# Optimization experiments

Hardware: AMD Instinct MI355X
Metric: run time of the kernel (lower is better)

## Reference

```python
import jax, jax.numpy as jnp
import numpy as np

H = 16  # num_heads
D = 1024  # hidden_dim
HD = D // H  # head_dim


def setup_inputs() -> dict:
    key = jax.random.key(0)
    ks = jax.random.split(key, 12)
    B, S = 2, 2048
    x = jax.random.normal(ks[0], (B, S, D), dtype=jnp.float32)
    attention_bias = jax.random.normal(ks[1], (H, S, S), dtype=jnp.float32) * 0.1
    # padding mask: True = masked; last (S - len) positions padded, no all-masked rows
    lengths = jax.random.randint(ks[2], (B,), S // 2, S + 1)
    key_padding_mask = jnp.arange(S)[None, :] >= lengths[:, None]  # [B, S] bool
    s = 1.0 / np.sqrt(D)
    Wq = jax.random.normal(ks[3], (D, D), dtype=jnp.float32) * s
    bq = jnp.zeros((D,), dtype=jnp.float32)
    Wk = jax.random.normal(ks[4], (D, D), dtype=jnp.float32) * s
    bk = jnp.zeros((D,), dtype=jnp.float32)
    Wv = jax.random.normal(ks[5], (D, D), dtype=jnp.float32) * s
    bv = jnp.zeros((D,), dtype=jnp.float32)
    Wo = jax.random.normal(ks[6], (D, D), dtype=jnp.float32) * s
    bo = jnp.zeros((D,), dtype=jnp.float32)
    return {"x": x, "attention_bias": attention_bias, "key_padding_mask": key_padding_mask,
            "Wq": Wq, "bq": bq, "Wk": Wk, "bk": bk, "Wv": Wv, "bv": bv, "Wo": Wo, "bo": bo}


def reference(x, attention_bias, key_padding_mask, Wq, bq, Wk, bk, Wv, bv, Wo, bo):
    B, S, _ = x.shape
    scale = HD ** (-0.5)

    def shape_heads(t):  # [B,S,D] -> [B,H,S,HD]
        return t.reshape(B, S, H, HD).transpose(0, 2, 1, 3)

    q = shape_heads(x @ Wq + bq)
    k = shape_heads(x @ Wk + bk)
    v = shape_heads(x @ Wv + bv)

    attn = jnp.einsum('bhqd,bhkd->bhqk', q, k) * scale  # [B,H,S,S]
    attn = attn + attention_bias[None]
    attn = jnp.where(key_padding_mask[:, None, None, :], -jnp.inf, attn)

    # handle fully-masked rows: zero their logits pre-softmax, zero weights after
    all_masked = jnp.all(key_padding_mask, axis=1)  # [B]
    bad = all_masked[:, None, None, None]
    safe_attn = jnp.where(bad, 0.0, attn)
    weights = jax.nn.softmax(safe_attn, axis=-1)
    weights = jnp.where(bad, 0.0, weights)

    context = jnp.einsum('bhqk,bhkd->bhqd', weights, v)  # [B,H,S,HD]
    context = context.transpose(0, 2, 1, 3).reshape(B, S, D)
    return context @ Wo + bo
```

## Files before the change

kernel.cpp:

```cpp
#include <hip/hip_runtime.h>
#include <hip/hip_bf16.h>
#include <stdint.h>

#define BB 2
#define SS 2048
#define DDIM 1024
#define HH 16
#define HDIM 64

typedef __hip_bfloat16 bf16;
typedef __bf16 bf16x8 __attribute__((ext_vector_type(8)));
typedef float f32x4 __attribute__((ext_vector_type(4)));
typedef short short8 __attribute__((ext_vector_type(8)));
typedef short s16x4 __attribute__((ext_vector_type(4)));

static __device__ __forceinline__ f32x4 mfma16(bf16x8 a, bf16x8 b, f32x4 c) {
  return __builtin_amdgcn_mfma_f32_16x16x32_bf16(a, b, c, 0, 0, 0);
}

static __device__ __forceinline__ void gload_lds16(const void* g, void* l) {
  __builtin_amdgcn_global_load_lds(
      (const __attribute__((address_space(1))) void*)g,
      (__attribute__((address_space(3))) void*)l, 16, 0, 0);
}

__global__ __launch_bounds__(256) void cvt_k(const float* __restrict__ src,
                                             bf16* __restrict__ dst) {
  const int base = (blockIdx.x * 256 + threadIdx.x) * 8;
  float4 a = *reinterpret_cast<const float4*>(src + base);
  float4 b = *reinterpret_cast<const float4*>(src + base + 4);
  union {
    bf16 h[8];
    short8 v;
  } u;
  u.h[0] = __float2bfloat16(a.x);
  u.h[1] = __float2bfloat16(a.y);
  u.h[2] = __float2bfloat16(a.z);
  u.h[3] = __float2bfloat16(a.w);
  u.h[4] = __float2bfloat16(b.x);
  u.h[5] = __float2bfloat16(b.y);
  u.h[6] = __float2bfloat16(b.z);
  u.h[7] = __float2bfloat16(b.w);
  *reinterpret_cast<short8*>(dst + base) = u.v;
}

__global__ __launch_bounds__(256) void transpose_cvt4_k(
    const float* __restrict__ s0, const float* __restrict__ s1,
    const float* __restrict__ s2, const float* __restrict__ s3,
    bf16* __restrict__ d0, bf16* __restrict__ d1, bf16* __restrict__ d2,
    bf16* __restrict__ d3) {
  __shared__ float tile[64][65];
  const int zi = blockIdx.z;
  const float* src = zi == 0 ? s0 : (zi == 1 ? s1 : (zi == 2 ? s2 : s3));
  bf16* dst = zi == 0 ? d0 : (zi == 1 ? d1 : (zi == 2 ? d2 : d3));
  const int t = threadIdx.x;
  const int r = t >> 2, c0 = (t & 3) * 16;
  const int bx = blockIdx.x * 64, by = blockIdx.y * 64;
  const float* sp = src + (size_t)(by + r) * DDIM + bx + c0;
#pragma unroll
  for (int j = 0; j < 16; ++j) tile[r][c0 + j] = sp[j];
  __syncthreads();
  bf16* dp = dst + (size_t)(bx + r) * DDIM + by + c0;
#pragma unroll
  for (int j = 0; j < 16; ++j) dp[j] = __float2bfloat16(tile[c0 + j][r]);
}

__global__ __launch_bounds__(64) void mask_pack_k(
    const int* __restrict__ kpm, unsigned long long* __restrict__ mb) {
  const int i = blockIdx.x;
  const int b = i >> 5, c = i & 31;
  const unsigned long long bits =
      __ballot(kpm[b * SS + c * 64 + threadIdx.x] != 0);
  if (threadIdx.x == 0) mb[i] = bits;
}

template <int MODE>
__global__ __launch_bounds__(256, 2) void gemm_bt(
    const bf16* __restrict__ A, const bf16* __restrict__ Bt,
    const float* __restrict__ b0, const float* __restrict__ b1,
    const float* __restrict__ b2, bf16* __restrict__ O0,
    bf16* __restrict__ O1, bf16* __restrict__ O2, float* __restrict__ Of) {
  constexpr int Kd = DDIM;
  __shared__ bf16x8 lA[128 * 8];
  __shared__ bf16x8 lB[128 * 8];
  const int tid = threadIdx.x;
  const int wave = tid >> 6, lane = tid & 63;
  const int l15 = lane & 15, l4 = lane >> 4;
  const int wm = wave >> 1, wn = wave & 1;
  const int m0 = blockIdx.x * 128, n0 = blockIdx.y * 128;
  const f32x4 z = {0.f, 0.f, 0.f, 0.f};
  f32x4 acc[4][4];
#pragma unroll
  for (int i = 0; i < 4; ++i)
#pragma unroll
    for (int j = 0; j < 4; ++j) acc[i][j] = z;

  for (int k0 = 0; k0 < Kd; k0 += 64) {
#pragma unroll
    for (int j = 0; j < 4; ++j) {
      const int slot = j * 256 + tid;
      const int r = slot >> 3, cs = slot & 7;
      const int c = cs ^ (r & 7);
      gload_lds16(A + (size_t)(m0 + r) * Kd + k0 + c * 8,
                  &lA[j * 256 + wave * 64]);
      gload_lds16(Bt + (size_t)(n0 + r) * Kd + k0 + c * 8,
                  &lB[j * 256 + wave * 64]);
    }
    __syncthreads();
    bf16x8 af[2][4], bfr[2][4];
#pragma unroll
    for (int ks = 0; ks < 2; ++ks) {
#pragma unroll
      for (int i = 0; i < 4; ++i) {
        const int ra = wm * 64 + i * 16 + l15;
        af[ks][i] = lA[ra * 8 + ((ks * 4 + l4) ^ (ra & 7))];
        const int rb = wn * 64 + i * 16 + l15;
        bfr[ks][i] = lB[rb * 8 + ((ks * 4 + l4) ^ (rb & 7))];
      }
    }
#pragma unroll
    for (int ks = 0; ks < 2; ++ks)
#pragma unroll
      for (int i = 0; i < 4; ++i)
#pragma unroll
        for (int j = 0; j < 4; ++j)
          acc[i][j] = mfma16(af[ks][i], bfr[ks][j], acc[i][j]);
    __syncthreads();
  }

#pragma unroll
  for (int i = 0; i < 4; ++i) {
    const int m = m0 + wm * 64 + i * 16 + l4 * 4;
#pragma unroll
    for (int j = 0; j < 4; ++j) {
      const int n = n0 + wn * 64 + j * 16 + l15;
      if (MODE == 1) {
        const float bb = b0[n];
#pragma unroll
        for (int r = 0; r < 4; ++r)
          Of[(size_t)(m + r) * DDIM + n] = acc[i][j][r] + bb;
      } else {
        const int sel = n >> 10, nn = n & 1023;
        const int h = nn >> 6, d = nn & 63;
        const float* bp = sel == 0 ? b0 : (sel == 1 ? b1 : b2);
        const float bb = bp[nn];
        const int b = m >> 11, s = m & 2047;
        if (sel == 2) {
          union {
            bf16 h4[4];
            s16x4 v;
          } u;
#pragma unroll
          for (int r = 0; r < 4; ++r)
            u.h4[r] = __float2bfloat16(acc[i][j][r] + bb);
          *reinterpret_cast<s16x4*>(
              &O2[((size_t)(b * HH + h) * HDIM + d) * SS + s]) = u.v;
        } else {
#pragma unroll
          for (int r = 0; r < 4; ++r) {
            const float val = acc[i][j][r] + bb;
            (sel ? O1 : O0)[((size_t)(b * HH + h) * SS + (s + r)) * HDIM + d] =
                __float2bfloat16(val);
          }
        }
      }
    }
  }
}

__global__ __launch_bounds__(512, 1) void attn_k(
    const bf16* __restrict__ Qb, const bf16* __restrict__ Kb,
    const bf16* __restrict__ Vt, const float* __restrict__ bias,
    const unsigned long long* __restrict__ mbits, bf16* __restrict__ ctx) {
  __shared__ bf16x8 lK[2][512];
  __shared__ bf16x8 lV[2][512];
  __shared__ unsigned int plP[8 * 512];
  const int tid = threadIdx.x;
  const int wave = tid >> 6, lane = tid & 63;
  const int l15 = lane & 15, l4 = lane >> 4;
  const int bid = ((blockIdx.x & 7) << 6) | (blockIdx.x >> 3);
  const int qblk = bid & 15, bh = bid >> 4;
  const int b = bh >> 4, h = bh & 15;
  const int q0b = qblk * 128;
  const int q0w = q0b + wave * 16;

  const bf16* Qp = Qb + ((size_t)bh * SS + q0w) * HDIM;
  const bf16* Kp = Kb + (size_t)bh * SS * HDIM;
  const bf16* Vp = Vt + (size_t)bh * HDIM * SS;
  const float* Bp = bias + (size_t)h * SS * SS + (size_t)(q0w + l15) * SS;
  unsigned int* plw = plP + wave * 512;

  const int rs0 = tid >> 3, cs0 = (tid & 7) ^ (rs0 & 7);

  gload_lds16(Kp + (size_t)rs0 * HDIM + cs0 * 8, &lK[0][wave * 64]);
  gload_lds16(Vp + (size_t)rs0 * SS + cs0 * 8, &lV[0][wave * 64]);

  f32x4 bA0 = *reinterpret_cast<const f32x4*>(Bp + 0 * 16 + l4 * 4);
  f32x4 bA1 = *reinterpret_cast<const f32x4*>(Bp + 1 * 16 + l4 * 4);
  f32x4 bA2 = *reinterpret_cast<const f32x4*>(Bp + 2 * 16 + l4 * 4);
  f32x4 bA3 = *reinterpret_cast<const f32x4*>(Bp + 3 * 16 + l4 * 4);
  f32x4 bB0 = bA0, bB1 = bA1, bB2 = bA2, bB3 = bA3;

  bf16x8 qf[2];
#pragma unroll
  for (int ks = 0; ks < 2; ++ks)
    qf[ks] = *reinterpret_cast<const bf16x8*>(Qp + (size_t)l15 * HDIM +
                                              ks * 32 + l4 * 8);
  const f32x4 z = {0.f, 0.f, 0.f, 0.f};
  f32x4 o[4];
#pragma unroll
  for (int dd = 0; dd < 4; ++dd) o[dd] = z;
  float mrow = -1e30f, lrow = 0.f;

  __syncthreads();

#define JJROW(JJ, BC)                                                     \
  {                                                                       \
    const unsigned nib = (unsigned)(mb >> ((JJ)*16 + l4 * 4)) & 15u;      \
    _Pragma("unroll") for (int r = 0; r < 4; ++r) {                       \
      const float a = ((nib >> r) & 1u) ? -1e30f : (BC)[r];               \
      v[JJ][r] = fmaf(sc[JJ][r], 0.125f, a);                              \
      bm = fmaxf(bm, v[JJ][r]);                                           \
    }                                                                     \
  }

#define STEP(T, BC0, BC1, BC2, BC3, BN0, BN1, BN2, BN3)                        \
  {                                                                            \
    const int cur = (T)&1;                                                     \
    const int nxt = cur ^ 1;                                                   \
    const int kbn = ((T) + 1) * 64;                                            \
    const bool pf = (T) < 31;                                                  \
    if (pf) {                                                                  \
      BN0 = *reinterpret_cast<const f32x4*>(Bp + kbn + 0 * 16 + l4 * 4);       \
      BN1 = *reinterpret_cast<const f32x4*>(Bp + kbn + 1 * 16 + l4 * 4);       \
      BN2 = *reinterpret_cast<const f32x4*>(Bp + kbn + 2 * 16 + l4 * 4);       \
      BN3 = *reinterpret_cast<const f32x4*>(Bp + kbn + 3 * 16 + l4 * 4);       \
    }                                                                          \
    f32x4 sc[4];                                                               \
    __builtin_amdgcn_s_setprio(1);                                             \
    _Pragma("unroll") for (int jj = 0; jj < 4; ++jj) {                         \
      const int R = jj * 16 + l15;                                             \
      bf16x8 kf0 = lK[cur][R * 8 + ((0 + l4) ^ (R & 7))];                      \
      bf16x8 kf1 = lK[cur][R * 8 + ((4 + l4) ^ (R & 7))];                      \
      f32x4 s = mfma16(kf0, qf[0], z);                                         \
      s = mfma16(kf1, qf[1], s);                                               \
      sc[jj] = s;                                                              \
    }                                                                          \
    __builtin_amdgcn_s_setprio(0);                                             \
    if (pf) {                            \
      gload_lds16(Kp + (size_t)(kbn + rs0) * HDIM + cs0 * 8,                   \
                  &lK[nxt][wave * 64]);                                        \
    }                                                                          \
    const unsigned long long mb = mbits[(b << 5) + (T)];                       \
    float v[4][4];                                                             \
    float bm = -1e30f;                                                         \
    JJROW(0, BC0)                                                              \
    JJROW(1, BC1)                                                              \
    JJROW(2, BC2)                                                              \
    JJROW(3, BC3)                                                              \
    bm = fmaxf(bm, __shfl_xor(bm, 16));                                        \
    bm = fmaxf(bm, __shfl_xor(bm, 32));                                        \
    const bool resc = __any(bm > mrow + 8.0f);                                 \
    float alpha = 1.0f;                                                        \
    if (resc) {                                                                \
      const float mn = fmaxf(mrow, bm);                                        \
      alpha = __expf(mrow - mn);                                               \
      mrow = mn;                                                               \
    }                                                                          \
    float ps = 0.f;                                                            \
    float p[4][4];                                                             \
    _Pragma("unroll") for (int jj = 0; jj < 4; ++jj)                           \
        _Pragma("unroll") for (int r = 0; r < 4; ++r) {                        \
      p[jj][r] = __expf(v[jj][r] - mrow);                                      \
      ps += p[jj][r];                                                          \
    }                                                                          \
    ps += __shfl_xor(ps, 16);                                                  \
    ps += __shfl_xor(ps, 32);                                                  \
    lrow = lrow * alpha + ps;                                                  \
    _Pragma("unroll") for (int jj = 0; jj < 4; ++jj) {                         \
      union {                                                                  \
        bf16 h4[4];                                                            \
        unsigned long long w;                                                  \
      } u;                                                                     \
      u.h4[0] = __float2bfloat16(p[jj][0]);                                    \
      u.h4[1] = __float2bfloat16(p[jj][1]);                                    \
      u.h4[2] = __float2bfloat16(p[jj][2]);                                    \
      u.h4[3] = __float2bfloat16(p[jj][3]);                                    \
      const int byte = (l15 * 128 + jj * 32 + l4 * 8) ^ ((l15 & 7) << 4);      \
      *reinterpret_cast<unsigned long long*>(                                  \
          reinterpret_cast<char*>(plw) + byte) = u.w;                          \
    }                                                                          \
    bf16x8 vfr[4][2];                                                          \
    _Pragma("unroll") for (int dd = 0; dd < 4; ++dd) {                         \
      const int D = dd * 16 + l15;                                             \
      vfr[dd][0] = lV[cur][D * 8 + ((0 + l4) ^ (D & 7))];                      \
      vfr[dd][1] = lV[cur][D * 8 + ((4 + l4) ^ (D & 7))];                      \
    }                                                                          \
    if (pf) {                            \
      gload_lds16(Vp + (size_t)rs0 * SS + kbn + cs0 * 8,                       \
                  &lV[nxt][wave * 64]);                                        \
    }                                                                          \
    asm volatile("s_waitcnt lgkmcnt(0)" ::: "memory");                         \
    bf16x8 pfr[2];                                                             \
    _Pragma("unroll") for (int ks = 0; ks < 2; ++ks) {                         \
      const int byte = (l15 * 128 + ks * 64 + l4 * 16) ^ ((l15 & 7) << 4);     \
      pfr[ks] = *reinterpret_cast<const bf16x8*>(                              \
          reinterpret_cast<const char*>(plw) + byte);                          \
    }                                                                          \
    if (resc) {                                                                \
      float ar0 = __shfl(alpha, l4 * 4 + 0);                                   \
      float ar1 = __shfl(alpha, l4 * 4 + 1);                                   \
      float ar2 = __shfl(alpha, l4 * 4 + 2);                                   \
      float ar3 = __shfl(alpha, l4 * 4 + 3);                                   \
      _Pragma("unroll") for (int dd = 0; dd < 4; ++dd) {                       \
        o[dd][0] *= ar0;                                                       \
        o[dd][1] *= ar1;                                                       \
        o[dd][2] *= ar2;                                                       \
        o[dd][3] *= ar3;                                                       \
      }                                                                        \
    }                                                                          \
    __builtin_amdgcn_s_setprio(1);                                             \
    _Pragma("unroll") for (int dd = 0; dd < 4; ++dd) {                         \
      o[dd] = mfma16(pfr[0], vfr[dd][0], o[dd]);                               \
      o[dd] = mfma16(pfr[1], vfr[dd][1], o[dd]);                               \
    }                                                                          \
    __builtin_amdgcn_s_setprio(0);                                             \
    __syncthreads();                                                           \
  }

  for (int t2 = 0; t2 < 16; ++t2) {
    const int te = t2 * 2;
    STEP(te, bA0, bA1, bA2, bA3, bB0, bB1, bB2, bB3)
    STEP(te + 1, bB0, bB1, bB2, bB3, bA0, bA1, bA2, bA3)
  }
#undef STEP
#undef JJROW

  const float rl = 1.0f / lrow;
  float rlr[4];
#pragma unroll
  for (int r = 0; r < 4; ++r) rlr[r] = __shfl(rl, l4 * 4 + r);
#pragma unroll
  for (int dd = 0; dd < 4; ++dd) {
#pragma unroll
    for (int r = 0; r < 4; ++r) {
      const float val = o[dd][r] * rlr[r];
      const int s = q0w + l4 * 4 + r;
      ctx[((size_t)b * SS + s) * DDIM + h * HDIM + dd * 16 + l15] =
          __float2bfloat16(val);
    }
  }
}

extern "C" void kernel_launch(void* const* d_in, const int* in_sizes, int n_in,
                              void* d_out, int out_size, void* d_ws,
                              size_t ws_size, hipStream_t stream) {
  const float* x = (const float*)d_in[0];
  const float* abias = (const float*)d_in[1];
  const int* kpm = (const int*)d_in[2];
  const float* Wq = (const float*)d_in[3];
  const float* bq = (const float*)d_in[4];
  const float* Wk = (const float*)d_in[5];
  const float* bk = (const float*)d_in[6];
  const float* Wv = (const float*)d_in[7];
  const float* bv = (const float*)d_in[8];
  const float* Wo = (const float*)d_in[9];
  const float* bo = (const float*)d_in[10];
  float* out = (float*)d_out;

  char* ws = (char*)d_ws;
  bf16* xb = (bf16*)ws;
  bf16* Wt = (bf16*)(ws + 8388608);
  bf16* Wot = (bf16*)(ws + 14680064);
  bf16* Qb = (bf16*)(ws + 16777216);
  bf16* Kb = (bf16*)(ws + 25165824);
  bf16* Vtb = (bf16*)(ws + 33554432);
  bf16* ctx = (bf16*)(ws + 41943040);
  unsigned long long* mbits =
      (unsigned long long*)(ws + 50331648);

  dim3 t256(256);
  cvt_k<<<dim3(2048), t256, 0, stream>>>(x, xb);
  transpose_cvt4_k<<<dim3(16, 16, 4), t256, 0, stream>>>(
      Wq, Wk, Wv, Wo, Wt, Wt + 1024 * 1024, Wt + 2 * 1024 * 1024, Wot);
  mask_pack_k<<<dim3(64), dim3(64), 0, stream>>>(kpm, mbits);

  gemm_bt<0><<<dim3(32, 24), t256, 0, stream>>>(xb, Wt, bq, bk, bv, Qb, Kb,
                                                Vtb, nullptr);
  attn_k<<<dim3(512), dim3(512), 0, stream>>>(Qb, Kb, Vtb, abias, mbits, ctx);
  gemm_bt<1><<<dim3(32, 8), t256, 0, stream>>>(ctx, Wot, bo, nullptr, nullptr,
                                               nullptr, nullptr, nullptr, out);
}
```

Measured before the change: 181.8 us.

## Issue K/V LDS prefetch at step start and relax end-of-step barrier wait

The attention loop now names its double buffers statically and issues the asynchronous global-to-LDS loads for the next K and V tiles at the top of each step, before the QK MFMAs, rather than partway through. The end-of-step __syncthreads is replaced by s_waitcnt vmcnt(4) plus a raw s_barrier. That wait only drains the two LDS-bound loads and leaves the four next-tile bias register loads in flight across the barrier. The aim is to hide more global-memory latency behind compute. It relies on vmcnt ordering being correct, and fewer registers are free while loads are outstanding.

```diff
diff --git a/kernel.cpp b/kernel.cpp
--- a/kernel.cpp
+++ b/kernel.cpp
@@ -172,8 +172,8 @@
     const bf16* __restrict__ Qb, const bf16* __restrict__ Kb,
     const bf16* __restrict__ Vt, const float* __restrict__ bias,
     const unsigned long long* __restrict__ mbits, bf16* __restrict__ ctx) {
-  __shared__ bf16x8 lK[2][512];
-  __shared__ bf16x8 lV[2][512];
+  __shared__ bf16x8 lK0[512], lK1[512];
+  __shared__ bf16x8 lV0[512], lV1[512];
   __shared__ unsigned int plP[8 * 512];
   const int tid = threadIdx.x;
   const int wave = tid >> 6, lane = tid & 63;
@@ -192,8 +192,8 @@
 
   const int rs0 = tid >> 3, cs0 = (tid & 7) ^ (rs0 & 7);
 
-  gload_lds16(Kp + (size_t)rs0 * HDIM + cs0 * 8, &lK[0][wave * 64]);
-  gload_lds16(Vp + (size_t)rs0 * SS + cs0 * 8, &lV[0][wave * 64]);
+  gload_lds16(Kp + (size_t)rs0 * HDIM + cs0 * 8, &lK0[wave * 64]);
+  gload_lds16(Vp + (size_t)rs0 * SS + cs0 * 8, &lV0[wave * 64]);
 
   f32x4 bA0 = *reinterpret_cast<const f32x4*>(Bp + 0 * 16 + l4 * 4);
   f32x4 bA1 = *reinterpret_cast<const f32x4*>(Bp + 1 * 16 + l4 * 4);
@@ -224,13 +224,13 @@
     }                                                                     \
   }
 
-#define STEP(T, BC0, BC1, BC2, BC3, BN0, BN1, BN2, BN3)                        \
+#define STEP(T, KC, KN, VC, VN, BC0, BC1, BC2, BC3, BN0, BN1, BN2, BN3)        \
   {                                                                            \
-    const int cur = (T)&1;                                                     \
-    const int nxt = cur ^ 1;                                                   \
     const int kbn = ((T) + 1) * 64;                                            \
     const bool pf = (T) < 31;                                                  \
-    if (pf) {                                                                  \
+    if (pf) {      \
+      gload_lds16(Kp + (size_t)(kbn + rs0) * HDIM + cs0 * 8, &KN[wave * 64]);  \
+      gload_lds16(Vp + (size_t)rs0 * SS + kbn + cs0 * 8, &VN[wave * 64]);      \
       BN0 = *reinterpret_cast<const f32x4*>(Bp + kbn + 0 * 16 + l4 * 4);       \
       BN1 = *reinterpret_cast<const f32x4*>(Bp + kbn + 1 * 16 + l4 * 4);       \
       BN2 = *reinterpret_cast<const f32x4*>(Bp + kbn + 2 * 16 + l4 * 4);       \
@@ -240,17 +240,13 @@
     __builtin_amdgcn_s_setprio(1);                                             \
     _Pragma("unroll") for (int jj = 0; jj < 4; ++jj) {                         \
       const int R = jj * 16 + l15;                                             \
-      bf16x8 kf0 = lK[cur][R * 8 + ((0 + l4) ^ (R & 7))];                      \
-      bf16x8 kf1 = lK[cur][R * 8 + ((4 + l4) ^ (R & 7))];                      \
+      bf16x8 kf0 = KC[R * 8 + ((0 + l4) ^ (R & 7))];                           \
+      bf16x8 kf1 = KC[R * 8 + ((4 + l4) ^ (R & 7))];                           \
       f32x4 s = mfma16(kf0, qf[0], z);                                         \
       s = mfma16(kf1, qf[1], s);                                               \
       sc[jj] = s;                                                              \
     }                                                                          \
     __builtin_amdgcn_s_setprio(0);                                             \
-    if (pf) {                            \
-      gload_lds16(Kp + (size_t)(kbn + rs0) * HDIM + cs0 * 8,                   \
-                  &lK[nxt][wave * 64]);                                        \
-    }                                                                          \
     const unsigned long long mb = mbits[(b << 5) + (T)];                       \
     float v[4][4];                                                             \
     float bm = -1e30f;                                                         \
@@ -293,12 +289,8 @@
     bf16x8 vfr[4][2];                                                          \
     _Pragma("unroll") for (int dd = 0; dd < 4; ++dd) {                         \
       const int D = dd * 16 + l15;                                             \
-      vfr[dd][0] = lV[cur][D * 8 + ((0 + l4) ^ (D & 7))];                      \
-      vfr[dd][1] = lV[cur][D * 8 + ((4 + l4) ^ (D & 7))];                      \
-    }                                                                          \
-    if (pf) {                            \
-      gload_lds16(Vp + (size_t)rs0 * SS + kbn + cs0 * 8,                       \
-                  &lV[nxt][wave * 64]);                                        \
+      vfr[dd][0] = VC[D * 8 + ((0 + l4) ^ (D & 7))];                           \
+      vfr[dd][1] = VC[D * 8 + ((4 + l4) ^ (D & 7))];                           \
     }                                                                          \
     asm volatile("s_waitcnt lgkmcnt(0)" ::: "memory");                         \
     bf16x8 pfr[2];                                                             \
@@ -325,13 +317,16 @@
       o[dd] = mfma16(pfr[1], vfr[dd][1], o[dd]);                               \
     }                                                                          \
     __builtin_amdgcn_s_setprio(0);                                             \
-    __syncthreads();                                                           \
+        \
+    asm volatile("s_waitcnt vmcnt(4)" ::: "memory");                           \
+    __builtin_amdgcn_sched_barrier(0);                                         \
+    __builtin_amdgcn_s_barrier();                                              \
   }
 
   for (int t2 = 0; t2 < 16; ++t2) {
     const int te = t2 * 2;
-    STEP(te, bA0, bA1, bA2, bA3, bB0, bB1, bB2, bB3)
-    STEP(te + 1, bB0, bB1, bB2, bB3, bA0, bA1, bA2, bA3)
+    STEP(te, lK0, lK1, lV0, lV1, bA0, bA1, bA2, bA3, bB0, bB1, bB2, bB3)
+    STEP(te + 1, lK1, lK0, lV1, lV0, bB0, bB1, bB2, bB3, bA0, bA1, bA2, bA3)
   }
 #undef STEP
 #undef JJROW
```

After: 206.8 us. 1.14x slower.

## Stage 128-key tiles in LDS to halve barrier count in attention loop

Applied to the files above, without the earlier changes.

The attention kernel now loads 128 keys of K and V into each LDS buffer instead of 64. It processes each tile as two 64-key halves and issues one __syncthreads per 128 keys rather than per 64. This cuts barrier and prefetch-issue overhead, at the cost of doubling LDS use for K/V and putting two async loads per buffer in flight. The V tile layout changes to 16 chunks per row with a matching swizzle.

```diff
diff --git a/kernel.cpp b/kernel.cpp
--- a/kernel.cpp
+++ b/kernel.cpp
@@ -172,8 +172,8 @@
     const bf16* __restrict__ Qb, const bf16* __restrict__ Kb,
     const bf16* __restrict__ Vt, const float* __restrict__ bias,
     const unsigned long long* __restrict__ mbits, bf16* __restrict__ ctx) {
-  __shared__ bf16x8 lK[2][512];
-  __shared__ bf16x8 lV[2][512];
+  __shared__ bf16x8 lK[2][1024];
+  __shared__ bf16x8 lV[2][1024];
   __shared__ unsigned int plP[8 * 512];
   const int tid = threadIdx.x;
   const int wave = tid >> 6, lane = tid & 63;
@@ -190,10 +190,14 @@
   const float* Bp = bias + (size_t)h * SS * SS + (size_t)(q0w + l15) * SS;
   unsigned int* plw = plP + wave * 512;
 
-  const int rs0 = tid >> 3, cs0 = (tid & 7) ^ (rs0 & 7);
-
-  gload_lds16(Kp + (size_t)rs0 * HDIM + cs0 * 8, &lK[0][wave * 64]);
-  gload_lds16(Vp + (size_t)rs0 * SS + cs0 * 8, &lV[0][wave * 64]);
+  const int krs = tid >> 3, kcs = (tid & 7) ^ (krs & 7);
+  const int vd = tid >> 4, vcs = (tid & 15) ^ (vd & 7);
+
+  gload_lds16(Kp + (size_t)krs * HDIM + kcs * 8, &lK[0][wave * 64]);
+  gload_lds16(Kp + (size_t)(64 + krs) * HDIM + kcs * 8,
+              &lK[0][512 + wave * 64]);
+  gload_lds16(Vp + (size_t)vd * SS + vcs * 8, &lV[0][wave * 64]);
+  gload_lds16(Vp + (size_t)(32 + vd) * SS + vcs * 8, &lV[0][512 + wave * 64]);
 
   f32x4 bA0 = *reinterpret_cast<const f32x4*>(Bp + 0 * 16 + l4 * 4);
   f32x4 bA1 = *reinterpret_cast<const f32x4*>(Bp + 1 * 16 + l4 * 4);
@@ -224,22 +228,19 @@
     }                                                                     \
   }
 
-#define STEP(T, BC0, BC1, BC2, BC3, BN0, BN1, BN2, BN3)                        \
+#define HALF(MW, KRO, KH, PF, KBN, BC0, BC1, BC2, BC3, BN0, BN1, BN2, BN3,     \
+             SG, KBS)                                                          \
   {                                                                            \
-    const int cur = (T)&1;                                                     \
-    const int nxt = cur ^ 1;                                                   \
-    const int kbn = ((T) + 1) * 64;                                            \
-    const bool pf = (T) < 31;                                                  \
-    if (pf) {                                                                  \
-      BN0 = *reinterpret_cast<const f32x4*>(Bp + kbn + 0 * 16 + l4 * 4);       \
-      BN1 = *reinterpret_cast<const f32x4*>(Bp + kbn + 1 * 16 + l4 * 4);       \
-      BN2 = *reinterpret_cast<const f32x4*>(Bp + kbn + 2 * 16 + l4 * 4);       \
-      BN3 = *reinterpret_cast<const f32x4*>(Bp + kbn + 3 * 16 + l4 * 4);       \
+    if (PF) {                                                                  \
+      BN0 = *reinterpret_cast<const f32x4*>(Bp + (KBN) + 0 * 16 + l4 * 4);     \
+      BN1 = *reinterpret_cast<const f32x4*>(Bp + (KBN) + 1 * 16 + l4 * 4);     \
+      BN2 = *reinterpret_cast<const f32x4*>(Bp + (KBN) + 2 * 16 + l4 * 4);     \
+      BN3 = *reinterpret_cast<const f32x4*>(Bp + (KBN) + 3 * 16 + l4 * 4);     \
     }                                                                          \
     f32x4 sc[4];                                                               \
     __builtin_amdgcn_s_setprio(1);                                             \
     _Pragma("unroll") for (int jj = 0; jj < 4; ++jj) {                         \
-      const int R = jj * 16 + l15;                                             \
+      const int R = (KRO) + jj * 16 + l15;                                     \
       bf16x8 kf0 = lK[cur][R * 8 + ((0 + l4) ^ (R & 7))];                      \
       bf16x8 kf1 = lK[cur][R * 8 + ((4 + l4) ^ (R & 7))];                      \
       f32x4 s = mfma16(kf0, qf[0], z);                                         \
@@ -247,11 +248,13 @@
       sc[jj] = s;                                                              \
     }                                                                          \
     __builtin_amdgcn_s_setprio(0);                                             \
-    if (pf) {                            \
-      gload_lds16(Kp + (size_t)(kbn + rs0) * HDIM + cs0 * 8,                   \
+    if (SG) {                       \
+      gload_lds16(Kp + (size_t)((KBS) + krs) * HDIM + kcs * 8,                 \
                   &lK[nxt][wave * 64]);                                        \
-    }                                                                          \
-    const unsigned long long mb = mbits[(b << 5) + (T)];                       \
+      gload_lds16(Kp + (size_t)((KBS) + 64 + krs) * HDIM + kcs * 8,            \
+                  &lK[nxt][512 + wave * 64]);                                  \
+    }                                                                          \
+    const unsigned long long mb = mbits[(b << 5) + (MW)];                      \
     float v[4][4];                                                             \
     float bm = -1e30f;                                                         \
     JJROW(0, BC0)                                                              \
@@ -293,12 +296,14 @@
     bf16x8 vfr[4][2];                                                          \
     _Pragma("unroll") for (int dd = 0; dd < 4; ++dd) {                         \
       const int D = dd * 16 + l15;                                             \
-      vfr[dd][0] = lV[cur][D * 8 + ((0 + l4) ^ (D & 7))];                      \
-      vfr[dd][1] = lV[cur][D * 8 + ((4 + l4) ^ (D & 7))];                      \
-    }                                                                          \
-    if (pf) {                            \
-      gload_lds16(Vp + (size_t)rs0 * SS + kbn + cs0 * 8,                       \
+      vfr[dd][0] = lV[cur][D * 16 + (((KH)*8 + 0 + l4) ^ (D & 7))];            \
+      vfr[dd][1] = lV[cur][D * 16 + (((KH)*8 + 4 + l4) ^ (D & 7))];            \
+    }                                                                          \
+    if (SG) {                       \
+      gload_lds16(Vp + (size_t)vd * SS + (KBS) + vcs * 8,                      \
                   &lV[nxt][wave * 64]);                                        \
+      gload_lds16(Vp + (size_t)(32 + vd) * SS + (KBS) + vcs * 8,               \
+                  &lV[nxt][512 + wave * 64]);                                  \
     }                                                                          \
     asm volatile("s_waitcnt lgkmcnt(0)" ::: "memory");                         \
     bf16x8 pfr[2];                                                             \
@@ -325,15 +330,20 @@
       o[dd] = mfma16(pfr[1], vfr[dd][1], o[dd]);                               \
     }                                                                          \
     __builtin_amdgcn_s_setprio(0);                                             \
-    __syncthreads();                                                           \
-  }
-
-  for (int t2 = 0; t2 < 16; ++t2) {
-    const int te = t2 * 2;
-    STEP(te, bA0, bA1, bA2, bA3, bB0, bB1, bB2, bB3)
-    STEP(te + 1, bB0, bB1, bB2, bB3, bA0, bA1, bA2, bA3)
-  }
-#undef STEP
+  }
+
+  for (int t = 0; t < 16; ++t) {
+    const int cur = t & 1;
+    const int nxt = cur ^ 1;
+    const int kb = t * 128;
+    const bool nl = t < 15;
+    HALF(2 * t, 0, 0, true, kb + 64, bA0, bA1, bA2, bA3, bB0, bB1, bB2, bB3,
+         false, 0)
+    HALF(2 * t + 1, 64, 1, nl, (kb + 128) & (SS - 1), bB0, bB1, bB2, bB3, bA0,
+         bA1, bA2, bA3, nl, kb + 128)
+    __syncthreads();
+  }
+#undef HALF
 #undef JJROW
 
   const float rl = 1.0f / lrow;
```

New measurement: 188.7 us. 1.04x slower.
